# Optimization experiments

Measured on AMD Instinct MI355X. Metric: run time of the kernel, lower is better.

## Reference

```python
import jax, jax.numpy as jnp
import numpy as np

H, N, SEQ = 256, 64, 4096

def setup_inputs() -> dict:
    key = jax.random.key(0)
    kA, kB, kC, kdt = jax.random.split(key, 4)
    W = jax.random.normal(kA, (H, N, N), dtype=jnp.float32)
    # Hurwitz (stable) A: skew-symmetric part minus 0.5*I, like HiPPO-style stable transitions
    A = 0.5 * (W - jnp.swapaxes(W, -1, -2)) - 0.5 * jnp.eye(N, dtype=jnp.float32)
    B = jax.random.normal(kB, (H, N), dtype=jnp.float32)
    C = jax.random.normal(kC, (H, N), dtype=jnp.float32)
    # log_dt around log(0.01), matching typical S4 timescale init
    log_dt = jax.random.normal(kdt, (H,), dtype=jnp.float32) * 0.5 + jnp.log(0.01)
    return {"A": A, "B": B, "C": C, "log_dt": log_dt, "L": SEQ}

def _bilinear(dt, A, B):
    # dt: (H,), A: (H,N,N), B: (H,N)
    n = A.shape[-1]
    I = jnp.eye(n, dtype=A.dtype)
    A_back = I - (dt[:, None, None] / 2) * A   # (H,N,N)
    A_fwd = I + (dt[:, None, None] / 2) * A    # (H,N,N)
    dA = jnp.linalg.solve(A_back, A_fwd)                       # (H,N,N)
    dB = dt[:, None] * jnp.linalg.solve(A_back, B[..., None])[..., 0]  # (H,N)
    return dA, dB

def _krylov(L, dA, dB, C):
    # K[h, l] = C[h] @ dA[h]^l @ dB[h], computed by squaring/doubling
    x = dB[..., None]  # (H, N, 1)
    A_ = dA
    while x.shape[-1] < L:
        x2 = jnp.einsum('hmn,hnl->hml', A_, x)  # apply current power
        x = jnp.concatenate([x, x2], axis=-1)
        if x.shape[-1] < L:
            A_ = jnp.einsum('hmn,hnk->hmk', A_, A_)  # square the power
    x = x[..., :L]  # (H, N, L)
    return jnp.einsum('hn,hnl->hl', C, x)  # (H, L)

def reference(A, B, C, log_dt, L):
    dt = jnp.exp(log_dt)
    dA, dB = _bilinear(dt, A, B)
    return _krylov(L, dA, dB, C)
```

## Files before the change

### kernel.cpp

```cpp
#include <hip/hip_runtime.h>

constexpr int STRU = 68;

typedef short v8s __attribute__((ext_vector_type(8)));
typedef float v4f __attribute__((ext_vector_type(4)));

__device__ __forceinline__ unsigned packhl(float x) {
    unsigned xb = __builtin_bit_cast(unsigned, x);
    unsigned hb = xb & 0xffff0000u;
    float lof = x - __builtin_bit_cast(float, hb);
    unsigned lb = __builtin_bit_cast(unsigned, lof) + 0x8000u;
    return __builtin_amdgcn_perm(xb, lb, 0x07060302u);
}

__device__ __forceinline__ float unpackf(unsigned v) {
    float h = __builtin_bit_cast(float, v & 0xffff0000u);
    float l = __builtin_bit_cast(float, v << 16);
    return h + l;
}

__device__ __forceinline__ void load_frag(const unsigned* p, v8s& hi, v8s& lo) {
    uint4 a = *(const uint4*)p;
    uint4 b = *(const uint4*)(p + 4);
    uint4 hw, lw;
    hw.x = __builtin_amdgcn_perm(a.y, a.x, 0x07060302u);
    hw.y = __builtin_amdgcn_perm(a.w, a.z, 0x07060302u);
    hw.z = __builtin_amdgcn_perm(b.y, b.x, 0x07060302u);
    hw.w = __builtin_amdgcn_perm(b.w, b.z, 0x07060302u);
    lw.x = __builtin_amdgcn_perm(a.y, a.x, 0x05040100u);
    lw.y = __builtin_amdgcn_perm(a.w, a.z, 0x05040100u);
    lw.z = __builtin_amdgcn_perm(b.y, b.x, 0x05040100u);
    lw.w = __builtin_amdgcn_perm(b.w, b.z, 0x05040100u);
    hi = __builtin_bit_cast(v8s, hw);
    lo = __builtin_bit_cast(v8s, lw);
}

#define MFMA16 __builtin_amdgcn_mfma_f32_16x16x32_bf16

template<int NT>
__device__ __forceinline__ void strip_acc(const unsigned* __restrict__ P,
                                          const unsigned* __restrict__ Q,
                                          int rb, int t0, int lane, v4f* acc) {
    const int nh = lane & 15, qd = lane >> 4;
    v8s ah[2], al[2];
    load_frag(P + (rb + nh) * STRU + qd * 8,      ah[0], al[0]);
    load_frag(P + (rb + nh) * STRU + 32 + qd * 8, ah[1], al[1]);
    v8s bh[NT][2], bl[NT][2];
    #pragma unroll
    for (int t = 0; t < NT; ++t) {
        const unsigned* qr = Q + ((t0 + t) * 16 + nh) * STRU;
        load_frag(qr + qd * 8,      bh[t][0], bl[t][0]);
        load_frag(qr + 32 + qd * 8, bh[t][1], bl[t][1]);
    }
    #pragma unroll
    for (int t = 0; t < NT; ++t) {
        v4f a0 = {0, 0, 0, 0}, a1 = {0, 0, 0, 0};
        #pragma unroll
        for (int kk = 0; kk < 2; ++kk) {
            a0 = MFMA16(ah[kk], bh[t][kk], a0, 0, 0, 0);
            a1 = MFMA16(ah[kk], bl[t][kk], a1, 0, 0, 0);
            a1 = MFMA16(al[kk], bh[t][kk], a1, 0, 0, 0);
        }
        acc[t] = a0 + a1;
    }
}

__launch_bounds__(512)
__global__ void krylov_kernel(const float* __restrict__ A,
                              const float* __restrict__ Bv,
                              const float* __restrict__ Cv,
                              const float* __restrict__ logdt,
                              float* __restrict__ out)
{
    const int h    = blockIdx.x;
    const int tid  = threadIdx.x;
    const int lane = tid & 63;
    const int w    = tid >> 6;
    const int nh   = lane & 15, qd = lane >> 4;

    __shared__ __align__(16) unsigned B0[64 * STRU], B1[64 * STRU], B2[64 * STRU],
                                      B3[64 * STRU], B4[64 * STRU], B5[64 * STRU];
    __shared__ float Bl[64], Cl[64], tmv[64];

    const float dt  = expf(logdt[h]);
    const float c   = 0.5f * dt;
    const float al  = 1.0f + 0.5f * c;
    const float sd2 = (c * c) / (al * al);
    const float c1  = 2.0f / al;
    const float c2  = 2.0f * c / (al * al);
    const float k1  = dt / al;
    const float k2  = dt * c / (al * al);

    const float* Ah = A + (size_t)h * 4096;

    for (int idx = tid; idx < 1024; idx += 512) {
        const int rr = idx >> 4, c0 = (idx & 15) * 4;
        float4 v = *(const float4*)(Ah + rr * 64 + c0);
        if (rr == c0 + 0) v.x += 0.5f;
        if (rr == c0 + 1) v.y += 0.5f;
        if (rr == c0 + 2) v.z += 0.5f;
        if (rr == c0 + 3) v.w += 0.5f;
        uint4 pk = make_uint4(packhl(v.x), packhl(v.y), packhl(v.z), packhl(v.w));
        *(uint4*)&B1[rr * STRU + c0] = pk;
    }
    if (tid < 64) Bl[tid] = Bv[h * 64 + tid];
    else if (tid < 128) Cl[tid - 64] = Cv[h * 64 + (tid - 64)];
    __syncthreads();

    const int hrb = 16 * (w & 3), ht0 = 2 * (w >> 2);

    {
        v4f a[2]; strip_acc<2>(B1, B1, hrb, ht0, lane, a);
        #pragma unroll
        for (int t = 0; t < 2; ++t)
            #pragma unroll
            for (int e = 0; e < 4; ++e) {
                const int row = hrb + 4 * qd + e, col = (ht0 + t) * 16 + nh;
                float dv = -sd2 * a[t][e];
                B3[row * STRU + col] = packhl(dv);
                B4[row * STRU + col] = packhl(dv + (row == col ? 1.0f : 0.0f));
            }
    }
    __syncthreads();
    {
        v4f a[2]; strip_acc<2>(B3, B4, hrb, ht0, lane, a);
        #pragma unroll
        for (int t = 0; t < 2; ++t)
            #pragma unroll
            for (int e = 0; e < 4; ++e) {
                const int row = hrb + 4 * qd + e, col = (ht0 + t) * 16 + nh;
                B5[row * STRU + col] = packhl(a[t][e] + (row == col ? 1.0f : 0.0f));
            }
    }
    __syncthreads();
    {
        v4f a[2]; strip_acc<2>(B3, B5, hrb, ht0, lane, a);
        #pragma unroll
        for (int t = 0; t < 2; ++t)
            #pragma unroll
            for (int e = 0; e < 4; ++e) {
                const int row = hrb + 4 * qd + e, col = (ht0 + t) * 16 + nh;
                B4[row * STRU + col] = packhl(a[t][e] + (row == col ? 1.0f : 0.0f));
            }
    }
    __syncthreads();
    {
        v4f a[2]; strip_acc<2>(B3, B4, hrb, ht0, lane, a);
        #pragma unroll
        for (int t = 0; t < 2; ++t)
            #pragma unroll
            for (int e = 0; e < 4; ++e) {
                const int row = hrb + 4 * qd + e, col = (ht0 + t) * 16 + nh;
                B5[row * STRU + col] = packhl(a[t][e] + (row == col ? 1.0f : 0.0f));
            }
    }
    __syncthreads();
    if (w < 4) {
        v4f a[4]; strip_acc<4>(B1, B5, 16 * w, 0, lane, a);
        #pragma unroll
        for (int t = 0; t < 4; ++t)
            #pragma unroll
            for (int e = 0; e < 4; ++e) {
                const int row = 16 * w + 4 * qd + e, col = t * 16 + nh;
                float tv = unpackf(B5[row * STRU + col]);
                float base = c1 * tv - (row == col ? 1.0f : 0.0f);
                float sv   = c2 * a[t][e];
                B0[row * STRU + col] = packhl(base + sv);
                B2[row * STRU + col] = packhl(base - sv);
            }
    } else if (w == 4) {
        float acc1 = 0.0f;
        #pragma unroll
        for (int m4 = 0; m4 < 16; ++m4) {
            uint4 tv = *(const uint4*)&B5[lane * STRU + 4 * m4];
            float4 b4 = *(const float4*)&Bl[4 * m4];
            acc1 += unpackf(tv.x) * b4.x + unpackf(tv.y) * b4.y
                  + unpackf(tv.z) * b4.z + unpackf(tv.w) * b4.w;
        }
        tmv[lane] = acc1;
        __threadfence_block();
        float acc2 = 0.0f;
        #pragma unroll
        for (int m4 = 0; m4 < 16; ++m4) {
            uint4 sv = *(const uint4*)&B1[lane * STRU + 4 * m4];
            float4 t4 = *(const float4*)&tmv[4 * m4];
            acc2 += unpackf(sv.x) * t4.x + unpackf(sv.y) * t4.y
                  + unpackf(sv.z) * t4.z + unpackf(sv.w) * t4.w;
        }
        B4[lane] = packhl(k1 * acc1 + k2 * acc2);
    }
    __syncthreads();

    unsigned *bX = B0, *bXT = B2, *bN = B1, *bNT = B3;
    #pragma unroll 1
    for (int p = 0; p < 12; ++p) {
        if (w < 4) {
            if (p < 11) {
                v4f a[4]; strip_acc<4>(bX, bXT, 16 * w, 0, lane, a);
                #pragma unroll
                for (int t = 0; t < 4; ++t) {
                    uint4 tp;
                    #pragma unroll
                    for (int e = 0; e < 4; ++e) {
                        unsigned pk = packhl(a[t][e]);
                        bN[(16 * w + 4 * qd + e) * STRU + t * 16 + nh] = pk;
                        ((unsigned*)&tp)[e] = pk;
                    }
                    *(uint4*)&bNT[(t * 16 + nh) * STRU + 16 * w + 4 * qd] = tp;
                }
            }
        } else {
            const bool isV = (p < 6);
            const int  k   = 1 << (isV ? p : p - 6);
            unsigned*  Kt  = isV ? B4 : B5;
            const unsigned* M = isV ? bX : bXT;
            const int ntr = (k + 15) >> 4;
            for (int tr = 0; tr < ntr; ++tr) {
                v4f a[1]; strip_acc<1>(Kt, M, tr * 16, w - 4, lane, a);
                #pragma unroll
                for (int e = 0; e < 4; ++e) {
                    const int j = tr * 16 + 4 * qd + e;
                    if (j < k) Kt[(k + j) * STRU + (w - 4) * 16 + nh] = packhl(a[0][e]);
                }
            }
            if (p == 0 && w == 4) B5[lane] = packhl(Cl[lane]);
        }
        __syncthreads();
        if (p < 11) {
            unsigned* t0_ = bX;  bX  = bN;  bN  = t0_;
            t0_ = bXT; bXT = bNT; bNT = t0_;
        }
    }

    {
        v4f a[2]; strip_acc<2>(B5, B4, hrb, ht0, lane, a);
        float* oh = out + (size_t)h * 4096;
        #pragma unroll
        for (int t = 0; t < 2; ++t)
            #pragma unroll
            for (int e = 0; e < 4; ++e)
                oh[(hrb + 4 * qd + e) * 64 + (ht0 + t) * 16 + nh] = a[t][e];
    }
}

extern "C" void kernel_launch(void* const* d_in, const int* in_sizes, int n_in,
                              void* d_out, int out_size, void* d_ws, size_t ws_size,
                              hipStream_t stream) {
    const float* A  = (const float*)d_in[0];
    const float* B  = (const float*)d_in[1];
    const float* C  = (const float*)d_in[2];
    const float* ld = (const float*)d_in[3];
    float* out = (float*)d_out;
    const int H = in_sizes[3];
    krylov_kernel<<<H, 512, 0, stream>>>(A, B, C, ld, out);
}
```

Baseline: 79.71 us.

## Split hi/lo bf16 planes and rebalance Krylov doubling work across all waves

Stores each matrix as two separate bf16 planes (hi and lo) instead of interleaved packed words, so MFMA fragments load directly without perm unpacking. The bilinear solve series is reorganised so two independent products run in the same stage, which removes one barrier. In the doubling loop all 8 waves now share the power-squaring work, and the Krylov extension runs on the first 2 or 4 waves instead of a separate half of the block. The first doubling step is folded into the setup stage. The cost is more scattered 16-bit LDS stores and a larger padded stride.

```diff
diff --git a/kernel.cpp b/kernel.cpp
--- a/kernel.cpp
+++ b/kernel.cpp
@@ -1,67 +1,78 @@
 #include <hip/hip_runtime.h>
-
-constexpr int STRU = 68;
 
 typedef short v8s __attribute__((ext_vector_type(8)));
 typedef float v4f __attribute__((ext_vector_type(4)));
-
-__device__ __forceinline__ unsigned packhl(float x) {
+typedef unsigned short u16;
+typedef unsigned short usv4 __attribute__((ext_vector_type(4)));
+
+constexpr int PSTR = 72;
+constexpr int PSZ  = 64 * PSTR;
+constexpr int MSZ  = 2 * PSZ;
+
+#define MFMA16 __builtin_amdgcn_mfma_f32_16x16x32_bf16
+
+__device__ __forceinline__ v8s ldf(const u16* plane, int row, int kc) {
+    return *(const v8s*)&plane[row * PSTR + kc];
+}
+
+__device__ __forceinline__ void split2(float x, u16& h, u16& l) {
     unsigned xb = __builtin_bit_cast(unsigned, x);
-    unsigned hb = xb & 0xffff0000u;
-    float lof = x - __builtin_bit_cast(float, hb);
+    h = (u16)(xb >> 16);
+    float lof = x - __builtin_bit_cast(float, xb & 0xffff0000u);
     unsigned lb = __builtin_bit_cast(unsigned, lof) + 0x8000u;
-    return __builtin_amdgcn_perm(xb, lb, 0x07060302u);
-}
-
-__device__ __forceinline__ float unpackf(unsigned v) {
-    float h = __builtin_bit_cast(float, v & 0xffff0000u);
-    float l = __builtin_bit_cast(float, v << 16);
-    return h + l;
-}
-
-__device__ __forceinline__ void load_frag(const unsigned* p, v8s& hi, v8s& lo) {
-    uint4 a = *(const uint4*)p;
-    uint4 b = *(const uint4*)(p + 4);
-    uint4 hw, lw;
-    hw.x = __builtin_amdgcn_perm(a.y, a.x, 0x07060302u);
-    hw.y = __builtin_amdgcn_perm(a.w, a.z, 0x07060302u);
-    hw.z = __builtin_amdgcn_perm(b.y, b.x, 0x07060302u);
-    hw.w = __builtin_amdgcn_perm(b.w, b.z, 0x07060302u);
-    lw.x = __builtin_amdgcn_perm(a.y, a.x, 0x05040100u);
-    lw.y = __builtin_amdgcn_perm(a.w, a.z, 0x05040100u);
-    lw.z = __builtin_amdgcn_perm(b.y, b.x, 0x05040100u);
-    lw.w = __builtin_amdgcn_perm(b.w, b.z, 0x05040100u);
-    hi = __builtin_bit_cast(v8s, hw);
-    lo = __builtin_bit_cast(v8s, lw);
-}
-
-#define MFMA16 __builtin_amdgcn_mfma_f32_16x16x32_bf16
-
-template<int NT>
-__device__ __forceinline__ void strip_acc(const unsigned* __restrict__ P,
-                                          const unsigned* __restrict__ Q,
-                                          int rb, int t0, int lane, v4f* acc) {
+    l = (u16)(lb >> 16);
+}
+__device__ __forceinline__ float join2(u16 h, u16 l) {
+    return __builtin_bit_cast(float, (unsigned)h << 16)
+         + __builtin_bit_cast(float, (unsigned)l << 16);
+}
+
+__device__ __forceinline__ void hstrip(const u16* __restrict__ P,
+                                       const u16* __restrict__ Q,
+                                       int rb, int cb, int lane, v4f acc[2]) {
     const int nh = lane & 15, qd = lane >> 4;
-    v8s ah[2], al[2];
-    load_frag(P + (rb + nh) * STRU + qd * 8,      ah[0], al[0]);
-    load_frag(P + (rb + nh) * STRU + 32 + qd * 8, ah[1], al[1]);
-    v8s bh[NT][2], bl[NT][2];
+    const int ar = rb + nh;
+    v8s ah0 = ldf(P, ar, qd * 8),       ah1 = ldf(P, ar, 32 + qd * 8);
+    v8s al0 = ldf(P + PSZ, ar, qd * 8), al1 = ldf(P + PSZ, ar, 32 + qd * 8);
     #pragma unroll
-    for (int t = 0; t < NT; ++t) {
-        const unsigned* qr = Q + ((t0 + t) * 16 + nh) * STRU;
-        load_frag(qr + qd * 8,      bh[t][0], bl[t][0]);
-        load_frag(qr + 32 + qd * 8, bh[t][1], bl[t][1]);
-    }
+    for (int t = 0; t < 2; ++t) {
+        const int br = cb + 16 * t + nh;
+        v8s bh0 = ldf(Q, br, qd * 8),       bh1 = ldf(Q, br, 32 + qd * 8);
+        v8s bl0 = ldf(Q + PSZ, br, qd * 8), bl1 = ldf(Q + PSZ, br, 32 + qd * 8);
+        v4f a0 = {0, 0, 0, 0}, a1 = {0, 0, 0, 0};
+        a0 = MFMA16(ah0, bh0, a0, 0, 0, 0);
+        a1 = MFMA16(ah0, bl0, a1, 0, 0, 0);
+        a1 = MFMA16(al0, bh0, a1, 0, 0, 0);
+        a0 = MFMA16(ah1, bh1, a0, 0, 0, 0);
+        a1 = MFMA16(ah1, bl1, a1, 0, 0, 0);
+        a1 = MFMA16(al1, bh1, a1, 0, 0, 0);
+        acc[t] = a0 + a1;
+    }
+}
+
+__device__ __forceinline__ void st2(u16* M, int row, int col, float v) {
+    u16 h, l; split2(v, h, l);
+    M[row * PSTR + col] = h;
+    M[PSZ + row * PSTR + col] = l;
+}
+
+__device__ __forceinline__ void st_dual(u16* Dr, u16* Dt, int rb, int cb,
+                                        int lane, const v4f acc[2]) {
+    const int nh = lane & 15, qd = lane >> 4;
     #pragma unroll
-    for (int t = 0; t < NT; ++t) {
-        v4f a0 = {0, 0, 0, 0}, a1 = {0, 0, 0, 0};
-        #pragma unroll
-        for (int kk = 0; kk < 2; ++kk) {
-            a0 = MFMA16(ah[kk], bh[t][kk], a0, 0, 0, 0);
-            a1 = MFMA16(ah[kk], bl[t][kk], a1, 0, 0, 0);
-            a1 = MFMA16(al[kk], bh[t][kk], a1, 0, 0, 0);
-        }
-        acc[t] = a0 + a1;
+    for (int t = 0; t < 2; ++t) {
+        const int col = cb + 16 * t + nh;
+        usv4 h4, l4;
+        #pragma unroll
+        for (int e = 0; e < 4; ++e) {
+            const int row = rb + 4 * qd + e;
+            u16 h, l; split2(acc[t][e], h, l);
+            Dr[row * PSTR + col] = h;
+            Dr[PSZ + row * PSTR + col] = l;
+            h4[e] = h; l4[e] = l;
+        }
+        *(usv4*)&Dt[col * PSTR + rb + 4 * qd] = h4;
+        *(usv4*)&Dt[PSZ + col * PSTR + rb + 4 * qd] = l4;
     }
 }
 
@@ -77,169 +88,179 @@
     const int lane = tid & 63;
     const int w    = tid >> 6;
     const int nh   = lane & 15, qd = lane >> 4;
-
-    __shared__ __align__(16) unsigned B0[64 * STRU], B1[64 * STRU], B2[64 * STRU],
-                                      B3[64 * STRU], B4[64 * STRU], B5[64 * STRU];
-    __shared__ float Bl[64], Cl[64], tmv[64];
+    const int rb   = 16 * (w >> 1), cb = 32 * (w & 1);
+
+    __shared__ __align__(16) u16 ARENA[6 * MSZ];
+    __shared__ float Bl[64], tmv[64];
+
+    u16* M0 = ARENA;
+    u16* M1 = ARENA + 1 * MSZ;
+    u16* M2 = ARENA + 2 * MSZ;
+    u16* M3 = ARENA + 3 * MSZ;
+    u16* M4 = ARENA + 4 * MSZ;
+    u16* M5 = ARENA + 5 * MSZ;
 
     const float dt  = expf(logdt[h]);
-    const float c   = 0.5f * dt;
-    const float al  = 1.0f + 0.5f * c;
-    const float sd2 = (c * c) / (al * al);
+    const float cc  = 0.5f * dt;
+    const float al  = 1.0f + 0.5f * cc;
+    const float sd2 = (cc * cc) / (al * al);
     const float c1  = 2.0f / al;
-    const float c2  = 2.0f * c / (al * al);
-    const float k1  = dt / al;
-    const float k2  = dt * c / (al * al);
+    const float c2  = 2.0f * cc / (al * al);
 
     const float* Ah = A + (size_t)h * 4096;
 
-    for (int idx = tid; idx < 1024; idx += 512) {
-        const int rr = idx >> 4, c0 = (idx & 15) * 4;
-        float4 v = *(const float4*)(Ah + rr * 64 + c0);
-        if (rr == c0 + 0) v.x += 0.5f;
-        if (rr == c0 + 1) v.y += 0.5f;
-        if (rr == c0 + 2) v.z += 0.5f;
-        if (rr == c0 + 3) v.w += 0.5f;
-        uint4 pk = make_uint4(packhl(v.x), packhl(v.y), packhl(v.z), packhl(v.w));
-        *(uint4*)&B1[rr * STRU + c0] = pk;
-    }
-    if (tid < 64) Bl[tid] = Bv[h * 64 + tid];
-    else if (tid < 128) Cl[tid - 64] = Cv[h * 64 + (tid - 64)];
-    __syncthreads();
-
-    const int hrb = 16 * (w & 3), ht0 = 2 * (w >> 2);
-
-    {
-        v4f a[2]; strip_acc<2>(B1, B1, hrb, ht0, lane, a);
-        #pragma unroll
-        for (int t = 0; t < 2; ++t)
-            #pragma unroll
-            for (int e = 0; e < 4; ++e) {
-                const int row = hrb + 4 * qd + e, col = (ht0 + t) * 16 + nh;
+    {
+        const int r0 = tid >> 3;
+        const int c0 = (tid & 7) * 8;
+        float xv[8];
+        *(float4*)&xv[0] = *(const float4*)(Ah + r0 * 64 + c0);
+        *(float4*)&xv[4] = *(const float4*)(Ah + r0 * 64 + c0 + 4);
+        const int dj = r0 - c0;
+        if (dj >= 0 && dj < 8) xv[dj] += 0.5f;
+        v8s vh, vl;
+        #pragma unroll
+        for (int j = 0; j < 8; ++j) {
+            u16 hh, ll; split2(xv[j], hh, ll);
+            vh[j] = (short)hh; vl[j] = (short)ll;
+        }
+        *(v8s*)&M0[r0 * PSTR + c0] = vh;
+        *(v8s*)&M0[PSZ + r0 * PSTR + c0] = vl;
+        if (tid < 64) Bl[tid] = Bv[h * 64 + tid];
+        else if (tid < 128) st2(M5, 0, tid - 64, Cv[h * 64 + (tid - 64)]);
+    }
+    __syncthreads();
+
+    {
+        v4f a[2]; hstrip(M0, M0, rb, cb, lane, a);
+        #pragma unroll
+        for (int t = 0; t < 2; ++t)
+            #pragma unroll
+            for (int e = 0; e < 4; ++e) {
+                const int row = rb + 4 * qd + e, col = cb + 16 * t + nh;
                 float dv = -sd2 * a[t][e];
-                B3[row * STRU + col] = packhl(dv);
-                B4[row * STRU + col] = packhl(dv + (row == col ? 1.0f : 0.0f));
-            }
-    }
-    __syncthreads();
-    {
-        v4f a[2]; strip_acc<2>(B3, B4, hrb, ht0, lane, a);
-        #pragma unroll
-        for (int t = 0; t < 2; ++t)
-            #pragma unroll
-            for (int e = 0; e < 4; ++e) {
-                const int row = hrb + 4 * qd + e, col = (ht0 + t) * 16 + nh;
-                B5[row * STRU + col] = packhl(a[t][e] + (row == col ? 1.0f : 0.0f));
-            }
-    }
-    __syncthreads();
-    {
-        v4f a[2]; strip_acc<2>(B3, B5, hrb, ht0, lane, a);
-        #pragma unroll
-        for (int t = 0; t < 2; ++t)
-            #pragma unroll
-            for (int e = 0; e < 4; ++e) {
-                const int row = hrb + 4 * qd + e, col = (ht0 + t) * 16 + nh;
-                B4[row * STRU + col] = packhl(a[t][e] + (row == col ? 1.0f : 0.0f));
-            }
-    }
-    __syncthreads();
-    {
-        v4f a[2]; strip_acc<2>(B3, B4, hrb, ht0, lane, a);
-        #pragma unroll
-        for (int t = 0; t < 2; ++t)
-            #pragma unroll
-            for (int e = 0; e < 4; ++e) {
-                const int row = hrb + 4 * qd + e, col = (ht0 + t) * 16 + nh;
-                B5[row * STRU + col] = packhl(a[t][e] + (row == col ? 1.0f : 0.0f));
-            }
-    }
-    __syncthreads();
-    if (w < 4) {
-        v4f a[4]; strip_acc<4>(B1, B5, 16 * w, 0, lane, a);
-        #pragma unroll
-        for (int t = 0; t < 4; ++t)
-            #pragma unroll
-            for (int e = 0; e < 4; ++e) {
-                const int row = 16 * w + 4 * qd + e, col = t * 16 + nh;
-                float tv = unpackf(B5[row * STRU + col]);
+                st2(M1, row, col, dv);
+                st2(M2, row, col, dv + (row == col ? 1.0f : 0.0f));
+            }
+    }
+    __syncthreads();
+    {
+        v4f a[2]; hstrip(M1, M2, rb, cb, lane, a);
+        #pragma unroll
+        for (int t = 0; t < 2; ++t)
+            #pragma unroll
+            for (int e = 0; e < 4; ++e)
+                st2(M3, rb + 4 * qd + e, cb + 16 * t + nh, a[t][e]);
+        v4f b[2]; hstrip(M1, M1, rb, cb, lane, b);
+        #pragma unroll
+        for (int t = 0; t < 2; ++t)
+            #pragma unroll
+            for (int e = 0; e < 4; ++e) {
+                const int row = rb + 4 * qd + e, col = cb + 16 * t + nh;
+                st2(M4, row, col, b[t][e] + (row == col ? 1.0f : 0.0f));
+            }
+    }
+    __syncthreads();
+    {
+        v4f a[2]; hstrip(M3, M4, rb, cb, lane, a);
+        #pragma unroll
+        for (int t = 0; t < 2; ++t)
+            #pragma unroll
+            for (int e = 0; e < 4; ++e) {
+                const int row = rb + 4 * qd + e, col = cb + 16 * t + nh;
+                st2(M2, row, col, a[t][e] + (row == col ? 1.0f : 0.0f));
+            }
+    }
+    __syncthreads();
+    {
+        v4f a[2]; hstrip(M0, M2, rb, cb, lane, a);
+        #pragma unroll
+        for (int t = 0; t < 2; ++t)
+            #pragma unroll
+            for (int e = 0; e < 4; ++e) {
+                const int row = rb + 4 * qd + e, col = cb + 16 * t + nh;
+                float tv = join2(M2[row * PSTR + col], M2[PSZ + row * PSTR + col]);
                 float base = c1 * tv - (row == col ? 1.0f : 0.0f);
                 float sv   = c2 * a[t][e];
-                B0[row * STRU + col] = packhl(base + sv);
-                B2[row * STRU + col] = packhl(base - sv);
-            }
-    } else if (w == 4) {
-        float acc1 = 0.0f;
-        #pragma unroll
-        for (int m4 = 0; m4 < 16; ++m4) {
-            uint4 tv = *(const uint4*)&B5[lane * STRU + 4 * m4];
-            float4 b4 = *(const float4*)&Bl[4 * m4];
-            acc1 += unpackf(tv.x) * b4.x + unpackf(tv.y) * b4.y
-                  + unpackf(tv.z) * b4.z + unpackf(tv.w) * b4.w;
-        }
-        tmv[lane] = acc1;
-        __threadfence_block();
-        float acc2 = 0.0f;
-        #pragma unroll
-        for (int m4 = 0; m4 < 16; ++m4) {
-            uint4 sv = *(const uint4*)&B1[lane * STRU + 4 * m4];
-            float4 t4 = *(const float4*)&tmv[4 * m4];
-            acc2 += unpackf(sv.x) * t4.x + unpackf(sv.y) * t4.y
-                  + unpackf(sv.z) * t4.z + unpackf(sv.w) * t4.w;
-        }
-        B4[lane] = packhl(k1 * acc1 + k2 * acc2);
-    }
-    __syncthreads();
-
-    unsigned *bX = B0, *bXT = B2, *bN = B1, *bNT = B3;
+                st2(M1, row, col, base + sv);
+                st2(M3, row, col, base - sv);
+            }
+    }
+    __syncthreads();
+
+    {
+        if (w < 4) {
+            v4f a[2]; hstrip(M3, M1, 16 * w, 0, lane, a);
+            st_dual(M2, M0, 16 * w, 0, lane, a);
+            v4f b[2]; hstrip(M3, M1, 16 * w, 32, lane, b);
+            st_dual(M2, M0, 16 * w, 32, lane, b);
+        } else if (w == 4) {
+            float acc1 = 0.f;
+            #pragma unroll
+            for (int m = 0; m < 8; ++m) {
+                v8s xh = ldf(M1, lane, m * 8);
+                v8s xl = ldf(M1 + PSZ, lane, m * 8);
+                #pragma unroll
+                for (int j = 0; j < 8; ++j)
+                    acc1 = fmaf(join2((u16)xh[j], (u16)xl[j]), Bl[m * 8 + j], acc1);
+            }
+            float v0 = cc * (acc1 + Bl[lane]);
+            tmv[lane] = v0;
+            __threadfence_block();
+            float acc2 = 0.f;
+            #pragma unroll
+            for (int m = 0; m < 8; ++m) {
+                v8s xh = ldf(M1, lane, m * 8);
+                v8s xl = ldf(M1 + PSZ, lane, m * 8);
+                #pragma unroll
+                for (int j = 0; j < 8; ++j)
+                    acc2 = fmaf(join2((u16)xh[j], (u16)xl[j]), tmv[m * 8 + j], acc2);
+            }
+            st2(M4, 0, lane, v0);
+            st2(M4, 1, lane, acc2);
+        }
+    }
+    __syncthreads();
+
+    u16 *pX = M0, *pXT = M2, *pXn = M1, *pXTn = M3;
     #pragma unroll 1
-    for (int p = 0; p < 12; ++p) {
-        if (w < 4) {
-            if (p < 11) {
-                v4f a[4]; strip_acc<4>(bX, bXT, 16 * w, 0, lane, a);
-                #pragma unroll
-                for (int t = 0; t < 4; ++t) {
-                    uint4 tp;
-                    #pragma unroll
-                    for (int e = 0; e < 4; ++e) {
-                        unsigned pk = packhl(a[t][e]);
-                        bN[(16 * w + 4 * qd + e) * STRU + t * 16 + nh] = pk;
-                        ((unsigned*)&tp)[e] = pk;
-                    }
-                    *(uint4*)&bNT[(t * 16 + nh) * STRU + 16 * w + 4 * qd] = tp;
-                }
-            }
-        } else {
-            const bool isV = (p < 6);
-            const int  k   = 1 << (isV ? p : p - 6);
-            unsigned*  Kt  = isV ? B4 : B5;
-            const unsigned* M = isV ? bX : bXT;
-            const int ntr = (k + 15) >> 4;
-            for (int tr = 0; tr < ntr; ++tr) {
-                v4f a[1]; strip_acc<1>(Kt, M, tr * 16, w - 4, lane, a);
+    for (int p = 1; p < 12; ++p) {
+        const bool isV = (p < 6);
+        const int  k   = 1 << (isV ? p : p - 6);
+        if (p < 11) {
+            v4f a[2];
+            if (isV) { hstrip(pXT, pX, rb, cb, lane, a); st_dual(pXTn, pXn, rb, cb, lane, a); }
+            else     { hstrip(pX, pXT, rb, cb, lane, a); st_dual(pXn, pXTn, rb, cb, lane, a); }
+        }
+        const int ndb = (k <= 16) ? 2 : 4;
+        if (w < ndb) {
+            const int sr = (k <= 16) ? 0 : (w >> 1);
+            const int ch = (k <= 16) ? w : (w & 1);
+            u16* Kt = isV ? M4 : M5;
+            const u16* Q = isV ? pX : pXT;
+            v4f a[2]; hstrip(Kt, Q, 16 * sr, 32 * ch, lane, a);
+            #pragma unroll
+            for (int t = 0; t < 2; ++t)
                 #pragma unroll
                 for (int e = 0; e < 4; ++e) {
-                    const int j = tr * 16 + 4 * qd + e;
-                    if (j < k) Kt[(k + j) * STRU + (w - 4) * 16 + nh] = packhl(a[0][e]);
+                    const int j = 16 * sr + 4 * qd + e;
+                    if (j < k) st2(Kt, k + j, 32 * ch + 16 * t + nh, a[t][e]);
                 }
-            }
-            if (p == 0 && w == 4) B5[lane] = packhl(Cl[lane]);
         }
         __syncthreads();
         if (p < 11) {
-            unsigned* t0_ = bX;  bX  = bN;  bN  = t0_;
-            t0_ = bXT; bXT = bNT; bNT = t0_;
-        }
-    }
-
-    {
-        v4f a[2]; strip_acc<2>(B5, B4, hrb, ht0, lane, a);
+            u16* s = pX;  pX  = pXn;  pXn  = s;
+            s = pXT; pXT = pXTn; pXTn = s;
+        }
+    }
+
+    {
+        v4f a[2]; hstrip(M5, M4, rb, cb, lane, a);
         float* oh = out + (size_t)h * 4096;
         #pragma unroll
         for (int t = 0; t < 2; ++t)
             #pragma unroll
             for (int e = 0; e < 4; ++e)
-                oh[(hrb + 4 * qd + e) * 64 + (ht0 + t) * 16 + nh] = a[t][e];
+                oh[(rb + 4 * qd + e) * 64 + cb + 16 * t + nh] = a[t][e];
     }
 }
 
```

After: 95.88 us. +20.3%, slower.

## Double block to 1024 threads and restructure bilinear solve and power loop

Applied to the files above, without the earlier changes.

Launches 1024 threads per head instead of 512 and redistributes MFMA tile work over 16 waves: the inverse-series setup overlaps computing the S² term with another product, the first squaring is folded into the setup phase, and the Krylov-column waves split their work across more waves. The dB computation is reformulated using dA rather than the inverse series. The aim is shorter per-phase critical paths and fewer barrier stages. In exchange, occupancy per CU is lower, larger barriers cost more, and register pressure under the 1024-thread launch bound may cause spills.

```diff
diff --git a/kernel.cpp b/kernel.cpp
--- a/kernel.cpp
+++ b/kernel.cpp
@@ -65,7 +65,7 @@
     }
 }
 
-__launch_bounds__(512)
+__launch_bounds__(1024)
 __global__ void krylov_kernel(const float* __restrict__ A,
                               const float* __restrict__ Bv,
                               const float* __restrict__ Cv,
@@ -77,169 +77,182 @@
     const int lane = tid & 63;
     const int w    = tid >> 6;
     const int nh   = lane & 15, qd = lane >> 4;
+    const int rb1  = 16 * (w >> 2), t01 = w & 3;
+    const int rb2  = 16 * (w >> 1), t02 = 2 * (w & 1);
 
     __shared__ __align__(16) unsigned B0[64 * STRU], B1[64 * STRU], B2[64 * STRU],
                                       B3[64 * STRU], B4[64 * STRU], B5[64 * STRU];
     __shared__ float Bl[64], Cl[64], tmv[64];
 
     const float dt  = expf(logdt[h]);
-    const float c   = 0.5f * dt;
-    const float al  = 1.0f + 0.5f * c;
-    const float sd2 = (c * c) / (al * al);
+    const float cc  = 0.5f * dt;
+    const float al  = 1.0f + 0.5f * cc;
+    const float sd2 = (cc * cc) / (al * al);
     const float c1  = 2.0f / al;
-    const float c2  = 2.0f * c / (al * al);
-    const float k1  = dt / al;
-    const float k2  = dt * c / (al * al);
+    const float c2  = 2.0f * cc / (al * al);
 
     const float* Ah = A + (size_t)h * 4096;
 
-    for (int idx = tid; idx < 1024; idx += 512) {
-        const int rr = idx >> 4, c0 = (idx & 15) * 4;
+    {
+        const int rr = tid >> 4, c0 = (tid & 15) * 4;
         float4 v = *(const float4*)(Ah + rr * 64 + c0);
         if (rr == c0 + 0) v.x += 0.5f;
         if (rr == c0 + 1) v.y += 0.5f;
         if (rr == c0 + 2) v.z += 0.5f;
         if (rr == c0 + 3) v.w += 0.5f;
         uint4 pk = make_uint4(packhl(v.x), packhl(v.y), packhl(v.z), packhl(v.w));
-        *(uint4*)&B1[rr * STRU + c0] = pk;
-    }
-    if (tid < 64) Bl[tid] = Bv[h * 64 + tid];
-    else if (tid < 128) Cl[tid - 64] = Cv[h * 64 + (tid - 64)];
-    __syncthreads();
-
-    const int hrb = 16 * (w & 3), ht0 = 2 * (w >> 2);
-
-    {
-        v4f a[2]; strip_acc<2>(B1, B1, hrb, ht0, lane, a);
+        *(uint4*)&B0[rr * STRU + c0] = pk;
+        if (tid < 64) Bl[tid] = Bv[h * 64 + tid];
+        else if (tid < 128) Cl[tid - 64] = Cv[h * 64 + (tid - 64)];
+    }
+    __syncthreads();
+
+    {
+        v4f a[1]; strip_acc<1>(B0, B0, rb1, t01, lane, a);
+        #pragma unroll
+        for (int e = 0; e < 4; ++e) {
+            const int row = rb1 + 4 * qd + e, col = t01 * 16 + nh;
+            float dv = -sd2 * a[0][e];
+            B3[row * STRU + col] = packhl(dv);
+            B4[row * STRU + col] = packhl(dv + (row == col ? 1.0f : 0.0f));
+        }
+    }
+    __syncthreads();
+    if (w < 8) {
+        v4f a[2]; strip_acc<2>(B3, B4, rb2, t02, lane, a);
         #pragma unroll
         for (int t = 0; t < 2; ++t)
             #pragma unroll
+            for (int e = 0; e < 4; ++e)
+                B5[(rb2 + 4 * qd + e) * STRU + (t02 + t) * 16 + nh] = packhl(a[t][e]);
+    } else {
+        const int rbu = 16 * ((w - 8) >> 1), tcu = 2 * ((w - 8) & 1);
+        v4f a[2]; strip_acc<2>(B3, B3, rbu, tcu, lane, a);
+        #pragma unroll
+        for (int t = 0; t < 2; ++t)
+            #pragma unroll
             for (int e = 0; e < 4; ++e) {
-                const int row = hrb + 4 * qd + e, col = (ht0 + t) * 16 + nh;
-                float dv = -sd2 * a[t][e];
-                B3[row * STRU + col] = packhl(dv);
-                B4[row * STRU + col] = packhl(dv + (row == col ? 1.0f : 0.0f));
-            }
-    }
-    __syncthreads();
-    {
-        v4f a[2]; strip_acc<2>(B3, B4, hrb, ht0, lane, a);
-        #pragma unroll
-        for (int t = 0; t < 2; ++t)
-            #pragma unroll
-            for (int e = 0; e < 4; ++e) {
-                const int row = hrb + 4 * qd + e, col = (ht0 + t) * 16 + nh;
-                B5[row * STRU + col] = packhl(a[t][e] + (row == col ? 1.0f : 0.0f));
-            }
-    }
-    __syncthreads();
-    {
-        v4f a[2]; strip_acc<2>(B3, B5, hrb, ht0, lane, a);
-        #pragma unroll
-        for (int t = 0; t < 2; ++t)
-            #pragma unroll
-            for (int e = 0; e < 4; ++e) {
-                const int row = hrb + 4 * qd + e, col = (ht0 + t) * 16 + nh;
-                B4[row * STRU + col] = packhl(a[t][e] + (row == col ? 1.0f : 0.0f));
-            }
-    }
-    __syncthreads();
-    {
-        v4f a[2]; strip_acc<2>(B3, B4, hrb, ht0, lane, a);
-        #pragma unroll
-        for (int t = 0; t < 2; ++t)
-            #pragma unroll
-            for (int e = 0; e < 4; ++e) {
-                const int row = hrb + 4 * qd + e, col = (ht0 + t) * 16 + nh;
-                B5[row * STRU + col] = packhl(a[t][e] + (row == col ? 1.0f : 0.0f));
-            }
-    }
-    __syncthreads();
-    if (w < 4) {
-        v4f a[4]; strip_acc<4>(B1, B5, 16 * w, 0, lane, a);
-        #pragma unroll
-        for (int t = 0; t < 4; ++t)
-            #pragma unroll
-            for (int e = 0; e < 4; ++e) {
-                const int row = 16 * w + 4 * qd + e, col = t * 16 + nh;
-                float tv = unpackf(B5[row * STRU + col]);
-                float base = c1 * tv - (row == col ? 1.0f : 0.0f);
-                float sv   = c2 * a[t][e];
-                B0[row * STRU + col] = packhl(base + sv);
-                B2[row * STRU + col] = packhl(base - sv);
-            }
-    } else if (w == 4) {
-        float acc1 = 0.0f;
-        #pragma unroll
-        for (int m4 = 0; m4 < 16; ++m4) {
-            uint4 tv = *(const uint4*)&B5[lane * STRU + 4 * m4];
-            float4 b4 = *(const float4*)&Bl[4 * m4];
-            acc1 += unpackf(tv.x) * b4.x + unpackf(tv.y) * b4.y
-                  + unpackf(tv.z) * b4.z + unpackf(tv.w) * b4.w;
-        }
-        tmv[lane] = acc1;
-        __threadfence_block();
-        float acc2 = 0.0f;
-        #pragma unroll
-        for (int m4 = 0; m4 < 16; ++m4) {
-            uint4 sv = *(const uint4*)&B1[lane * STRU + 4 * m4];
-            float4 t4 = *(const float4*)&tmv[4 * m4];
-            acc2 += unpackf(sv.x) * t4.x + unpackf(sv.y) * t4.y
-                  + unpackf(sv.z) * t4.z + unpackf(sv.w) * t4.w;
-        }
-        B4[lane] = packhl(k1 * acc1 + k2 * acc2);
-    }
-    __syncthreads();
-
-    unsigned *bX = B0, *bXT = B2, *bN = B1, *bNT = B3;
+                const int row = rbu + 4 * qd + e, col = (tcu + t) * 16 + nh;
+                B2[row * STRU + col] = packhl(a[t][e] + (row == col ? 1.0f : 0.0f));
+            }
+    }
+    __syncthreads();
+    {
+        v4f a[1]; strip_acc<1>(B5, B2, rb1, t01, lane, a);
+        #pragma unroll
+        for (int e = 0; e < 4; ++e) {
+            const int row = rb1 + 4 * qd + e, col = t01 * 16 + nh;
+            B4[row * STRU + col] = packhl(a[0][e] + (row == col ? 1.0f : 0.0f));
+        }
+    }
+    __syncthreads();
+    {
+        v4f a[1]; strip_acc<1>(B0, B4, rb1, t01, lane, a);
+        #pragma unroll
+        for (int e = 0; e < 4; ++e) {
+            const int row = rb1 + 4 * qd + e, col = t01 * 16 + nh;
+            float tv = unpackf(B4[row * STRU + col]);
+            float base = c1 * tv - (row == col ? 1.0f : 0.0f);
+            float sv   = c2 * a[0][e];
+            B1[row * STRU + col] = packhl(base + sv);
+            B2[row * STRU + col] = packhl(base - sv);
+        }
+    }
+    __syncthreads();
+    {
+        if (w < 8) {
+            v4f a[2]; strip_acc<2>(B1, B2, rb2, t02, lane, a);
+            #pragma unroll
+            for (int t = 0; t < 2; ++t) {
+                uint4 tp;
+                #pragma unroll
+                for (int e = 0; e < 4; ++e) {
+                    unsigned pk = packhl(a[t][e]);
+                    B3[(rb2 + 4 * qd + e) * STRU + (t02 + t) * 16 + nh] = pk;
+                    ((unsigned*)&tp)[e] = pk;
+                }
+                *(uint4*)&B0[((t02 + t) * 16 + nh) * STRU + rb2 + 4 * qd] = tp;
+            }
+        } else if (w == 8) {
+            float acc1 = 0.0f;
+            #pragma unroll
+            for (int m4 = 0; m4 < 16; ++m4) {
+                uint4 xv = *(const uint4*)&B1[lane * STRU + 4 * m4];
+                float4 b4 = *(const float4*)&Bl[4 * m4];
+                acc1 += unpackf(xv.x) * b4.x + unpackf(xv.y) * b4.y
+                      + unpackf(xv.z) * b4.z + unpackf(xv.w) * b4.w;
+            }
+            float v0 = cc * (acc1 + Bl[lane]);
+            tmv[lane] = v0;
+            __threadfence_block();
+            float acc2 = 0.0f;
+            #pragma unroll
+            for (int m4 = 0; m4 < 16; ++m4) {
+                uint4 xv = *(const uint4*)&B1[lane * STRU + 4 * m4];
+                float4 t4 = *(const float4*)&tmv[4 * m4];
+                acc2 += unpackf(xv.x) * t4.x + unpackf(xv.y) * t4.y
+                      + unpackf(xv.z) * t4.z + unpackf(xv.w) * t4.w;
+            }
+            B4[0 * STRU + lane] = packhl(v0);
+            B4[1 * STRU + lane] = packhl(acc2);
+        } else if (w == 9) {
+            B5[lane] = packhl(Cl[lane]);
+        }
+    }
+    __syncthreads();
+
+    unsigned *bX = B3, *bXT = B0, *bN = B1, *bNT = B2;
     #pragma unroll 1
-    for (int p = 0; p < 12; ++p) {
-        if (w < 4) {
+    for (int p = 1; p < 12; ++p) {
+        if (w < 8) {
             if (p < 11) {
-                v4f a[4]; strip_acc<4>(bX, bXT, 16 * w, 0, lane, a);
+                v4f a[2]; strip_acc<2>(bX, bXT, rb2, t02, lane, a);
                 #pragma unroll
-                for (int t = 0; t < 4; ++t) {
+                for (int t = 0; t < 2; ++t) {
                     uint4 tp;
                     #pragma unroll
                     for (int e = 0; e < 4; ++e) {
                         unsigned pk = packhl(a[t][e]);
-                        bN[(16 * w + 4 * qd + e) * STRU + t * 16 + nh] = pk;
+                        bN[(rb2 + 4 * qd + e) * STRU + (t02 + t) * 16 + nh] = pk;
                         ((unsigned*)&tp)[e] = pk;
                     }
-                    *(uint4*)&bNT[(t * 16 + nh) * STRU + 16 * w + 4 * qd] = tp;
+                    *(uint4*)&bNT[((t02 + t) * 16 + nh) * STRU + rb2 + 4 * qd] = tp;
                 }
             }
         } else {
             const bool isV = (p < 6);
             const int  k   = 1 << (isV ? p : p - 6);
-            unsigned*  Kt  = isV ? B4 : B5;
-            const unsigned* M = isV ? bX : bXT;
-            const int ntr = (k + 15) >> 4;
-            for (int tr = 0; tr < ntr; ++tr) {
-                v4f a[1]; strip_acc<1>(Kt, M, tr * 16, w - 4, lane, a);
+            const int  nd  = (k > 16) ? 4 : 2;
+            const int  u   = w - 8;
+            if (u < nd) {
+                const int sr = (k > 16) ? (u >> 1) : 0;
+                const int ch = (k > 16) ? (u & 1) : u;
+                unsigned* Kt = isV ? B4 : B5;
+                const unsigned* Mq = isV ? bX : bXT;
+                v4f a[2]; strip_acc<2>(Kt, Mq, 16 * sr, 2 * ch, lane, a);
                 #pragma unroll
-                for (int e = 0; e < 4; ++e) {
-                    const int j = tr * 16 + 4 * qd + e;
-                    if (j < k) Kt[(k + j) * STRU + (w - 4) * 16 + nh] = packhl(a[0][e]);
-                }
-            }
-            if (p == 0 && w == 4) B5[lane] = packhl(Cl[lane]);
+                for (int t = 0; t < 2; ++t)
+                    #pragma unroll
+                    for (int e = 0; e < 4; ++e) {
+                        const int j = 16 * sr + 4 * qd + e;
+                        if (j < k)
+                            Kt[(k + j) * STRU + (2 * ch + t) * 16 + nh] = packhl(a[t][e]);
+                    }
+            }
         }
         __syncthreads();
         if (p < 11) {
-            unsigned* t0_ = bX;  bX  = bN;  bN  = t0_;
-            t0_ = bXT; bXT = bNT; bNT = t0_;
-        }
-    }
-
-    {
-        v4f a[2]; strip_acc<2>(B5, B4, hrb, ht0, lane, a);
+            unsigned* s = bX;  bX  = bN;  bN  = s;
+            s = bXT; bXT = bNT; bNT = s;
+        }
+    }
+
+    {
+        v4f a[1]; strip_acc<1>(B5, B4, rb1, t01, lane, a);
         float* oh = out + (size_t)h * 4096;
         #pragma unroll
-        for (int t = 0; t < 2; ++t)
-            #pragma unroll
-            for (int e = 0; e < 4; ++e)
-                oh[(hrb + 4 * qd + e) * 64 + (ht0 + t) * 16 + nh] = a[t][e];
+        for (int e = 0; e < 4; ++e)
+            oh[(rb1 + 4 * qd + e) * 64 + t01 * 16 + nh] = a[0][e];
     }
 }
 
@@ -252,5 +265,5 @@
     const float* ld = (const float*)d_in[3];
     float* out = (float*)d_out;
     const int H = in_sizes[3];
-    krylov_kernel<<<H, 512, 0, stream>>>(A, B, C, ld, out);
-}
+    krylov_kernel<<<H, 1024, 0, stream>>>(A, B, C, ld, out);
+}
```

Result: slower. 82.00 us (+2.9%).
